# Optimization experiments

Hardware: AMD Instinct MI355X
Metric: run time of the kernel (lower is better)

Reference implementation:

```python
import jax, jax.numpy as jnp
import numpy as np

T, H, I, BS = 512, 4096, 11008, 128


def _dequant(w, scale, bs):
    # w: [I, H], scale: [I//bs, H//bs] -> w * blockwise-broadcast scale
    Iw, Hw = w.shape
    wb = w.reshape(Iw // bs, bs, Hw // bs, bs)
    return (wb * scale[:, None, :, None]).reshape(Iw, Hw)


def setup_inputs() -> dict:
    key = jax.random.key(0)
    ks = jax.random.split(key, 7)
    return {
        "x": jax.random.normal(ks[0], (T, H), dtype=jnp.float32),
        "gate_weight": jax.random.normal(ks[1], (I, H), dtype=jnp.float32) * 0.02,
        "up_weight": jax.random.normal(ks[2], (I, H), dtype=jnp.float32) * 0.02,
        "down_weight": jax.random.normal(ks[3], (I, H), dtype=jnp.float32) * 0.02,
        "gate_scale": jax.random.uniform(ks[4], (I // BS, H // BS), dtype=jnp.float32),
        "up_scale": jax.random.uniform(ks[5], (I // BS, H // BS), dtype=jnp.float32),
        "down_scale": jax.random.uniform(ks[6], (I // BS, H // BS), dtype=jnp.float32),
        "blocksize": BS,
    }


def reference(x, gate_weight, up_weight, down_weight, gate_scale, up_scale, down_scale, blocksize):
    # Block-dequantize the three quantized weights, then SwiGLU MLP:
    # out = (silu(x @ Wg^T) * (x @ Wu^T)) @ Wd   (Wd stored pre-transposed as [I, H])
    wg = _dequant(gate_weight, gate_scale, blocksize)  # [I, H]
    wu = _dequant(up_weight, up_scale, blocksize)      # [I, H]
    wd = _dequant(down_weight, down_scale, blocksize)  # [I, H]
    gate = jnp.einsum('th,ih->ti', x, wg)  # [T, I]
    up = jnp.einsum('th,ih->ti', x, wu)    # [T, I]
    h = jax.nn.silu(gate) * up             # [T, I]
    return jnp.einsum('ti,ih->th', h, wd)  # [T, H]
```

## Files before the change

kernel.cpp:

```cpp
#include <hip/hip_runtime.h>
#include <hip/hip_bf16.h>
#include <cstdint>
#include <cstddef>

#define T_DIM 512
#define H_DIM 4096
#define I_DIM 11008
#define KSPLIT 4

typedef __bf16 bf16_t;
typedef bf16_t bf16x8 __attribute__((ext_vector_type(8)));
typedef float f32x4 __attribute__((ext_vector_type(4)));
typedef unsigned short us16;
typedef us16 us16x8 __attribute__((ext_vector_type(8)));
typedef us16 us16x4 __attribute__((ext_vector_type(4)));

__device__ __forceinline__ us16 f2bf(float f) {
    union { float f; uint32_t u; } v; v.f = f;
    uint32_t u = v.u;
    return (us16)((u + 0x7FFFu + ((u >> 16) & 1u)) >> 16);
}

__device__ __forceinline__ uint32_t pkbf(float a, float b) {
    __hip_bfloat162 h = __float22bfloat162_rn(make_float2(a, b));
    uint32_t u;
    __builtin_memcpy(&u, &h, 4);
    return u;
}

__device__ __forceinline__ f32x4 mfma16(us16x8 a, us16x8 b, f32x4 c) {
    return __builtin_amdgcn_mfma_f32_16x16x32_bf16(
        __builtin_bit_cast(bf16x8, a), __builtin_bit_cast(bf16x8, b), c, 0, 0, 0);
}

__device__ __forceinline__ void gload_lds16(const us16* g, us16* l) {
    __builtin_amdgcn_global_load_lds(
        (const __attribute__((address_space(1))) void*)g,
        (__attribute__((address_space(3))) void*)l, 16, 0, 0);
}

__global__ void cvt_x_kernel(const float* __restrict__ x, us16* __restrict__ xb) {
    int idx = (blockIdx.x * 256 + threadIdx.x) * 8;
    float4 a = *(const float4*)(x + idx);
    float4 b = *(const float4*)(x + idx + 4);
    us16x8 v;
    v[0] = f2bf(a.x); v[1] = f2bf(a.y); v[2] = f2bf(a.z); v[3] = f2bf(a.w);
    v[4] = f2bf(b.x); v[5] = f2bf(b.y); v[6] = f2bf(b.z); v[7] = f2bf(b.w);
    *(us16x8*)(xb + idx) = v;
}

__global__ __launch_bounds__(256) void trans_wd(
    const float* __restrict__ wd, const float* __restrict__ sd, us16* __restrict__ wdt)
{
    const int t   = threadIdx.x;
    const int bid = blockIdx.x;
    const int bi  = bid % (I_DIM / 256);
    const int bh  = bid / (I_DIM / 256);
    const int i   = bi * 256 + t;
    const int h0  = bh * 16;
    const float s = sd[(i >> 7) * (H_DIM / 128) + (h0 >> 7)];
    const float* src = wd + (size_t)i * H_DIM + h0;
    float4 v0 = *(const float4*)(src + 0);
    float4 v1 = *(const float4*)(src + 4);
    float4 v2 = *(const float4*)(src + 8);
    float4 v3 = *(const float4*)(src + 12);
    us16 o[16];
    o[0]=f2bf(v0.x*s); o[1]=f2bf(v0.y*s); o[2]=f2bf(v0.z*s); o[3]=f2bf(v0.w*s);
    o[4]=f2bf(v1.x*s); o[5]=f2bf(v1.y*s); o[6]=f2bf(v1.z*s); o[7]=f2bf(v1.w*s);
    o[8]=f2bf(v2.x*s); o[9]=f2bf(v2.y*s); o[10]=f2bf(v2.z*s); o[11]=f2bf(v2.w*s);
    o[12]=f2bf(v3.x*s); o[13]=f2bf(v3.y*s); o[14]=f2bf(v3.z*s); o[15]=f2bf(v3.w*s);
    #pragma unroll
    for (int j = 0; j < 16; ++j)
        wdt[(size_t)(h0 + j) * I_DIM + i] = o[j];
}

__global__ __launch_bounds__(256, 3) void gemm1_fused(
    const us16*  __restrict__ xb,
    const float* __restrict__ wg,
    const float* __restrict__ wu,
    const float* __restrict__ sgArr,
    const float* __restrict__ suArr,
    us16*        __restrict__ hbuf)
{
    __shared__ us16 As [128 * 72];
    __shared__ us16 Bgs[64 * 72];
    __shared__ us16 Bus[64 * 72];

    const int t   = threadIdx.x;
    const int bid = blockIdx.x;
    const int bm  = bid & 3;
    const int bn  = bid >> 2;
    const int m0  = bm * 128, n0 = bn * 64;

    const int w = t >> 6, l = t & 63;
    const int q = l >> 4, r = l & 15;
    const int m_off = (w >> 1) * 64, n_off = (w & 1) * 32;

    const int ar[4] = { t >> 3, (t + 256) >> 3, (t + 512) >> 3, (t + 768) >> 3 };
    const int ac    = (t & 7) * 8;
    const int br[4] = { t >> 4, (t + 256) >> 4, (t + 512) >> 4, (t + 768) >> 4 };
    const int bc    = (t & 15) * 4;

    f32x4 accg[4][2], accu[4][2];
    #pragma unroll
    for (int m = 0; m < 4; ++m)
        #pragma unroll
        for (int n = 0; n < 2; ++n) {
            accg[m][n] = f32x4{0.f,0.f,0.f,0.f};
            accu[m][n] = f32x4{0.f,0.f,0.f,0.f};
        }

    us16x8 ab[4];
    float4 gb[4], ub[4];

    {
        const int k0 = 0;
        #pragma unroll
        for (int p = 0; p < 4; ++p)
            ab[p] = *(const us16x8*)(xb + (size_t)(m0 + ar[p]) * H_DIM + k0 + ac);
        #pragma unroll
        for (int p = 0; p < 4; ++p) {
            gb[p] = *(const float4*)(wg + (size_t)(n0 + br[p]) * H_DIM + k0 + bc);
            ub[p] = *(const float4*)(wu + (size_t)(n0 + br[p]) * H_DIM + k0 + bc);
        }
    }

    for (int kt = 0; kt < H_DIM / 64; ++kt) {
        const float sg = sgArr[(bn >> 1) * (H_DIM / 128) + (kt >> 1)];
        const float su = suArr[(bn >> 1) * (H_DIM / 128) + (kt >> 1)];

        __builtin_amdgcn_s_barrier();

        #pragma unroll
        for (int p = 0; p < 4; ++p)
            *(us16x8*)(As + ar[p] * 72 + ac) = ab[p];
        #pragma unroll
        for (int p = 0; p < 4; ++p) {
            uint2 vg, vu;
            vg.x = pkbf(gb[p].x * sg, gb[p].y * sg);
            vg.y = pkbf(gb[p].z * sg, gb[p].w * sg);
            vu.x = pkbf(ub[p].x * su, ub[p].y * su);
            vu.y = pkbf(ub[p].z * su, ub[p].w * su);
            *(uint2*)(Bgs + br[p] * 72 + bc) = vg;
            *(uint2*)(Bus + br[p] * 72 + bc) = vu;
        }

        {
            const int kn = ((kt + 1) & 63) * 64;
            #pragma unroll
            for (int p = 0; p < 4; ++p)
                ab[p] = *(const us16x8*)(xb + (size_t)(m0 + ar[p]) * H_DIM + kn + ac);
            #pragma unroll
            for (int p = 0; p < 4; ++p) {
                gb[p] = *(const float4*)(wg + (size_t)(n0 + br[p]) * H_DIM + kn + bc);
                ub[p] = *(const float4*)(wu + (size_t)(n0 + br[p]) * H_DIM + kn + bc);
            }
        }

        __builtin_amdgcn_s_waitcnt(0xC07F);
        __builtin_amdgcn_s_barrier();

        #pragma unroll
        for (int ks = 0; ks < 2; ++ks) {
            us16x8 af[4], bg[2], bu[2];
            #pragma unroll
            for (int m = 0; m < 4; ++m)
                af[m] = *(const us16x8*)(As + (m_off + m * 16 + r) * 72 + ks * 32 + q * 8);
            #pragma unroll
            for (int n = 0; n < 2; ++n) {
                bg[n] = *(const us16x8*)(Bgs + (n_off + n * 16 + r) * 72 + ks * 32 + q * 8);
                bu[n] = *(const us16x8*)(Bus + (n_off + n * 16 + r) * 72 + ks * 32 + q * 8);
            }
            #pragma unroll
            for (int m = 0; m < 4; ++m)
                #pragma unroll
                for (int n = 0; n < 2; ++n) {
                    accg[m][n] = mfma16(af[m], bg[n], accg[m][n]);
                    accu[m][n] = mfma16(af[m], bu[n], accu[m][n]);
                }
        }
    }

    #pragma unroll
    for (int m = 0; m < 4; ++m)
        #pragma unroll
        for (int n = 0; n < 2; ++n)
            #pragma unroll
            for (int rr = 0; rr < 4; ++rr) {
                int grow = m0 + m_off + m * 16 + q * 4 + rr;
                int gcol = n0 + n_off + n * 16 + r;
                float g = accg[m][n][rr];
                float u = accu[m][n][rr];
                float hv = (g / (1.0f + __expf(-g))) * u;
                hbuf[(size_t)grow * I_DIM + gcol] = f2bf(hv);
            }
}

template <bool USE_PART>
__global__ __launch_bounds__(256, 2) void gemm2_splitk(
    const us16* __restrict__ hbuf,
    const us16* __restrict__ wdt,
    float*      __restrict__ outp)
{
    __shared__ us16 As[128 * 32];
    __shared__ us16 Bs[128 * 32];

    const int t   = threadIdx.x;
    const int bid = blockIdx.x;
    const int bm  = bid & 3;
    const int bn  = (bid >> 2) & 31;
    const int bk  = bid >> 7;
    const int m0  = bm * 128, n0 = bn * 128;
    const int kbase = bk * (I_DIM / KSPLIT);

    const int w = t >> 6, l = t & 63;
    const int q = l >> 4, r = l & 15;
    const int m_off = (w >> 1) * 64, n_off = (w & 1) * 64;

    const int arow = w * 16 + (l >> 2);
    const int acol = (l & 3) * 8;

    f32x4 acc[4][4];
    #pragma unroll
    for (int m = 0; m < 4; ++m)
        #pragma unroll
        for (int n = 0; n < 4; ++n) acc[m][n] = f32x4{0.f,0.f,0.f,0.f};

    for (int kt = 0; kt < (I_DIM / KSPLIT) / 32; ++kt) {
        const int k0 = kbase + kt * 32;
        #pragma unroll
        for (int p = 0; p < 2; ++p) {
            gload_lds16(hbuf + (size_t)(m0 + p * 64 + arow) * I_DIM + k0 + acol,
                        As + (p * 64 + w * 16) * 32);
            gload_lds16(wdt + (size_t)(n0 + p * 64 + arow) * I_DIM + k0 + acol,
                        Bs + (p * 64 + w * 16) * 32);
        }
        __syncthreads();

        us16x8 af[4], bfr[4];
        #pragma unroll
        for (int m = 0; m < 4; ++m)
            af[m] = *(const us16x8*)(As + (m_off + m * 16 + r) * 32 + q * 8);
        #pragma unroll
        for (int n = 0; n < 4; ++n)
            bfr[n] = *(const us16x8*)(Bs + (n_off + n * 16 + r) * 32 + q * 8);
        #pragma unroll
        for (int m = 0; m < 4; ++m)
            #pragma unroll
            for (int n = 0; n < 4; ++n)
                acc[m][n] = mfma16(af[m], bfr[n], acc[m][n]);
        __syncthreads();
    }

    float* base = USE_PART ? outp + (size_t)bk * T_DIM * H_DIM : outp;
    #pragma unroll
    for (int m = 0; m < 4; ++m)
        #pragma unroll
        for (int n = 0; n < 4; ++n)
            #pragma unroll
            for (int rr = 0; rr < 4; ++rr) {
                int grow = m0 + m_off + m * 16 + q * 4 + rr;
                int gcol = n0 + n_off + n * 16 + r;
                if (USE_PART)
                    base[(size_t)grow * H_DIM + gcol] = acc[m][n][rr];
                else
                    atomicAdd(&base[(size_t)grow * H_DIM + gcol], acc[m][n][rr]);
            }
}

__global__ void reduce4_kernel(const float* __restrict__ part, float* __restrict__ out) {
    const size_t i = ((size_t)blockIdx.x * 256 + threadIdx.x) * 4;
    const size_t S = (size_t)T_DIM * H_DIM;
    float4 a = *(const float4*)(part + i);
    float4 b = *(const float4*)(part + S + i);
    float4 c = *(const float4*)(part + 2 * S + i);
    float4 d = *(const float4*)(part + 3 * S + i);
    float4 o;
    o.x = a.x + b.x + c.x + d.x;
    o.y = a.y + b.y + c.y + d.y;
    o.z = a.z + b.z + c.z + d.z;
    o.w = a.w + b.w + c.w + d.w;
    *(float4*)(out + i) = o;
}

extern "C" void kernel_launch(void* const* d_in, const int* in_sizes, int n_in,
                              void* d_out, int out_size, void* d_ws, size_t ws_size,
                              hipStream_t stream) {
    const float* x  = (const float*)d_in[0];
    const float* wg = (const float*)d_in[1];
    const float* wu = (const float*)d_in[2];
    const float* wd = (const float*)d_in[3];
    const float* sg = (const float*)d_in[4];
    const float* su = (const float*)d_in[5];
    const float* sd = (const float*)d_in[6];
    float* out = (float*)d_out;

    const size_t xb_bytes   = (size_t)T_DIM * H_DIM * 2;
    const size_t hb_bytes   = (size_t)T_DIM * I_DIM * 2;
    const size_t wdt_bytes  = (size_t)H_DIM * I_DIM * 2;
    const size_t part_bytes = (size_t)KSPLIT * T_DIM * H_DIM * 4;

    us16*  xb   = (us16*)d_ws;
    us16*  hb   = (us16*)((char*)d_ws + xb_bytes);
    us16*  wdt  = (us16*)((char*)d_ws + xb_bytes + hb_bytes);
    float* part = (float*)((char*)d_ws + xb_bytes + hb_bytes + wdt_bytes);

    cvt_x_kernel<<<(T_DIM * H_DIM) / (256 * 8), 256, 0, stream>>>(x, xb);
    gemm1_fused<<<(I_DIM / 64) * (T_DIM / 128), 256, 0, stream>>>(xb, wg, wu, sg, su, hb);
    trans_wd<<<(I_DIM / 256) * (H_DIM / 16), 256, 0, stream>>>(wd, sd, wdt);

    if (ws_size >= xb_bytes + hb_bytes + wdt_bytes + part_bytes) {
        gemm2_splitk<true><<<(T_DIM / 128) * (H_DIM / 128) * KSPLIT, 256, 0, stream>>>(hb, wdt, part);
        reduce4_kernel<<<(T_DIM * H_DIM) / (256 * 4), 256, 0, stream>>>(part, out);
    } else {
        (void)hipMemsetAsync(out, 0, (size_t)T_DIM * H_DIM * sizeof(float), stream);
        gemm2_splitk<false><<<(T_DIM / 128) * (H_DIM / 128) * KSPLIT, 256, 0, stream>>>(hb, wdt, out);
    }
}
```

Before: 727.6 us.

## Double-buffer gemm1 register prefetch and remap block IDs for XCD locality

After: 1.311 ms. 1.8x slower.

```diff
diff --git a/kernel.cpp b/kernel.cpp
--- a/kernel.cpp
+++ b/kernel.cpp
@@ -86,11 +86,12 @@
     __shared__ us16 Bgs[64 * 72];
     __shared__ us16 Bus[64 * 72];
 
-    const int t   = threadIdx.x;
-    const int bid = blockIdx.x;
-    const int bm  = bid & 3;
-    const int bn  = bid >> 2;
-    const int m0  = bm * 128, n0 = bn * 64;
+    const int t    = threadIdx.x;
+    const int bid  = blockIdx.x;
+    const int wgid = (bid & 7) * 86 + (bid >> 3);
+    const int bm   = wgid & 3;
+    const int bn   = wgid >> 2;
+    const int m0   = bm * 128, n0 = bn * 64;
 
     const int w = t >> 6, l = t & 63;
     const int q = l >> 4, r = l & 15;
@@ -101,6 +102,8 @@
     const int br[4] = { t >> 4, (t + 256) >> 4, (t + 512) >> 4, (t + 768) >> 4 };
     const int bc    = (t & 15) * 4;
 
+    const int sRow  = (bn >> 1) * (H_DIM / 128);
+
     f32x4 accg[4][2], accu[4][2];
     #pragma unroll
     for (int m = 0; m < 4; ++m)
@@ -110,50 +113,110 @@
             accu[m][n] = f32x4{0.f,0.f,0.f,0.f};
         }
 
-    us16x8 ab[4];
-    float4 gb[4], ub[4];
-
-    {
-        const int k0 = 0;
+    us16x8 ab0[4], ab1[4];
+    float4 gb0[4], ub0[4], gb1[4], ub1[4];
+
+    #pragma unroll
+    for (int p = 0; p < 4; ++p) {
+        ab0[p] = *(const us16x8*)(xb + (size_t)(m0 + ar[p]) * H_DIM + 0  + ac);
+        ab1[p] = *(const us16x8*)(xb + (size_t)(m0 + ar[p]) * H_DIM + 64 + ac);
+    }
+    #pragma unroll
+    for (int p = 0; p < 4; ++p) {
+        gb0[p] = *(const float4*)(wg + (size_t)(n0 + br[p]) * H_DIM + 0  + bc);
+        ub0[p] = *(const float4*)(wu + (size_t)(n0 + br[p]) * H_DIM + 0  + bc);
+        gb1[p] = *(const float4*)(wg + (size_t)(n0 + br[p]) * H_DIM + 64 + bc);
+        ub1[p] = *(const float4*)(wu + (size_t)(n0 + br[p]) * H_DIM + 64 + bc);
+    }
+
+    float sg_c = sgArr[sRow];
+    float su_c = suArr[sRow];
+
+    for (int kt = 0; kt < H_DIM / 64; kt += 2) {
+        const int ki = kt >> 1;
+        const float sg = sg_c, su = su_c;
+        {
+            const int kn = (ki + 1) & 31;
+            sg_c = sgArr[sRow + kn];
+            su_c = suArr[sRow + kn];
+        }
+
+        __builtin_amdgcn_s_barrier();
+
         #pragma unroll
         for (int p = 0; p < 4; ++p)
-            ab[p] = *(const us16x8*)(xb + (size_t)(m0 + ar[p]) * H_DIM + k0 + ac);
-        #pragma unroll
-        for (int p = 0; p < 4; ++p) {
-            gb[p] = *(const float4*)(wg + (size_t)(n0 + br[p]) * H_DIM + k0 + bc);
-            ub[p] = *(const float4*)(wu + (size_t)(n0 + br[p]) * H_DIM + k0 + bc);
-        }
-    }
-
-    for (int kt = 0; kt < H_DIM / 64; ++kt) {
-        const float sg = sgArr[(bn >> 1) * (H_DIM / 128) + (kt >> 1)];
-        const float su = suArr[(bn >> 1) * (H_DIM / 128) + (kt >> 1)];
-
-        __builtin_amdgcn_s_barrier();
-
-        #pragma unroll
-        for (int p = 0; p < 4; ++p)
-            *(us16x8*)(As + ar[p] * 72 + ac) = ab[p];
+            *(us16x8*)(As + ar[p] * 72 + ac) = ab0[p];
         #pragma unroll
         for (int p = 0; p < 4; ++p) {
             uint2 vg, vu;
-            vg.x = pkbf(gb[p].x * sg, gb[p].y * sg);
-            vg.y = pkbf(gb[p].z * sg, gb[p].w * sg);
-            vu.x = pkbf(ub[p].x * su, ub[p].y * su);
-            vu.y = pkbf(ub[p].z * su, ub[p].w * su);
+            vg.x = pkbf(gb0[p].x * sg, gb0[p].y * sg);
+            vg.y = pkbf(gb0[p].z * sg, gb0[p].w * sg);
+            vu.x = pkbf(ub0[p].x * su, ub0[p].y * su);
+            vu.y = pkbf(ub0[p].z * su, ub0[p].w * su);
             *(uint2*)(Bgs + br[p] * 72 + bc) = vg;
             *(uint2*)(Bus + br[p] * 72 + bc) = vu;
         }
 
         {
-            const int kn = ((kt + 1) & 63) * 64;
+            const int kn = ((kt + 2) & 63) * 64;
             #pragma unroll
             for (int p = 0; p < 4; ++p)
-                ab[p] = *(const us16x8*)(xb + (size_t)(m0 + ar[p]) * H_DIM + kn + ac);
+                ab0[p] = *(const us16x8*)(xb + (size_t)(m0 + ar[p]) * H_DIM + kn + ac);
             #pragma unroll
             for (int p = 0; p < 4; ++p) {
-                gb[p] = *(const float4*)(wg + (size_t)(n0 + br[p]) * H_DIM + kn + bc);
-                ub[p] = *(const float4*)(wu + (size_t)(n0 + br[p]) * H_DIM + kn + bc);
+                gb0[p] = *(const float4*)(wg + (size_t)(n0 + br[p]) * H_DIM + kn + bc);
+                ub0[p] = *(const float4*)(wu + (size_t)(n0 + br[p]) * H_DIM + kn + bc);
+            }
+        }
+
+        __builtin_amdgcn_s_waitcnt(0xC07F);
+        __builtin_amdgcn_s_barrier();
+
+        #pragma unroll
+        for (int ks = 0; ks < 2; ++ks) {
+            us16x8 af[4], bg[2], bu[2];
+            #pragma unroll
+            for (int m = 0; m < 4; ++m)
+                af[m] = *(const us16x8*)(As + (m_off + m * 16 + r) * 72 + ks * 32 + q * 8);
+            #pragma unroll
+            for (int n = 0; n < 2; ++n) {
+                bg[n] = *(const us16x8*)(Bgs + (n_off + n * 16 + r) * 72 + ks * 32 + q * 8);
+                bu[n] = *(const us16x8*)(Bus + (n_off + n * 16 + r) * 72 + ks * 32 + q * 8);
+            }
+            #pragma unroll
+            for (int m = 0; m < 4; ++m)
+                #pragma unroll
+                for (int n = 0; n < 2; ++n) {
+                    accg[m][n] = mfma16(af[m], bg[n], accg[m][n]);
+                    accu[m][n] = mfma16(af[m], bu[n], accu[m][n]);
+                }
+        }
+
+        __builtin_amdgcn_s_barrier();
+
+        #pragma unroll
+        for (int p = 0; p < 4; ++p)
+            *(us16x8*)(As + ar[p] * 72 + ac) = ab1[p];
+        #pragma unroll
+        for (int p = 0; p < 4; ++p) {
+            uint2 vg, vu;
+            vg.x = pkbf(gb1[p].x * sg, gb1[p].y * sg);
+            vg.y = pkbf(gb1[p].z * sg, gb1[p].w * sg);
+            vu.x = pkbf(ub1[p].x * su, ub1[p].y * su);
+            vu.y = pkbf(ub1[p].z * su, ub1[p].w * su);
+            *(uint2*)(Bgs + br[p] * 72 + bc) = vg;
+            *(uint2*)(Bus + br[p] * 72 + bc) = vu;
+        }
+
+        {
+            const int kn = ((kt + 3) & 63) * 64;
+            #pragma unroll
+            for (int p = 0; p < 4; ++p)
+                ab1[p] = *(const us16x8*)(xb + (size_t)(m0 + ar[p]) * H_DIM + kn + ac);
+            #pragma unroll
+            for (int p = 0; p < 4; ++p) {
+                gb1[p] = *(const float4*)(wg + (size_t)(n0 + br[p]) * H_DIM + kn + bc);
+                ub1[p] = *(const float4*)(wu + (size_t)(n0 + br[p]) * H_DIM + kn + bc);
             }
         }
 
@@ -207,9 +270,12 @@
 
     const int t   = threadIdx.x;
     const int bid = blockIdx.x;
-    const int bm  = bid & 3;
-    const int bn  = (bid >> 2) & 31;
-    const int bk  = bid >> 7;
+    const int x   = bid & 7;
+    const int j   = bid >> 3;
+    const int bm  = j & 3;
+    const int g   = x * 16 + (j >> 2);
+    const int bn  = g & 31;
+    const int bk  = g >> 5;
     const int m0  = bm * 128, n0 = bn * 128;
     const int kbase = bk * (I_DIM / KSPLIT);
 
```
